# Optimization experiments

Measured on AMD Instinct MI355X. Metric: run time of the kernel, lower is better.

The kernel has to match this reference:

```python
import jax, jax.numpy as jnp
import numpy as np

B, C = 2000000, 24

def setup_inputs() -> dict:
    key = jax.random.key(0)
    k1, k2 = jax.random.split(key)
    input = jax.random.normal(k1, (B, C), dtype=jnp.float32)
    target = jax.random.randint(k2, (B, C), 0, 2, dtype=jnp.int32)
    return {"input": input, "target": target}

def reference(input, target):
    # LSEP: loss = log1p( sum_i sum_{p in pos_i, n in neg_i} exp(x_in - x_ip) ) / B
    # The ragged double loop factorizes per row:
    #   sum_{p,n} exp(x_n - x_p) = (sum_n exp(x_n)) * (sum_p exp(-x_p))
    pos = target > 0
    neg = target == 0
    s_neg = jnp.sum(jnp.where(neg, jnp.exp(input), 0.0), axis=1)   # [B]
    s_pos = jnp.sum(jnp.where(pos, jnp.exp(-input), 0.0), axis=1)  # [B]
    total = jnp.sum(s_neg * s_pos)
    batch_size = input.shape[0]
    return jnp.log1p(total) / batch_size
```

## Files before the change

### kernel.cpp

```cpp
#include <hip/hip_runtime.h>
#include <math.h>


constexpr int  ROWS    = 2000000;
constexpr int  HALVES  = ROWS * 2;
constexpr int  BLOCK   = 256;
constexpr int  GRID    = 3125;
constexpr int  THREADS = GRID * BLOCK;
constexpr int  ITERS   = HALVES / THREADS;

__global__ __launch_bounds__(BLOCK, 4) void lsep_main(
        const float4* __restrict__ input,
        const int4*   __restrict__ target,
        double*       __restrict__ partials)
{
    const int tid = blockIdx.x * BLOCK + threadIdx.x;

    double acc = 0.0;

    float4 xa0, xa1, xa2; int4 ta0, ta1, ta2;
    {
        const int f = 3 * tid;
        xa0 = input[f];  xa1 = input[f + 1];  xa2 = input[f + 2];
        ta0 = target[f]; ta1 = target[f + 1]; ta2 = target[f + 2];
    }

    int h = tid;
    #pragma unroll
    for (int i = 0; i < ITERS; ++i) {
        float4 xb0, xb1, xb2; int4 tb0, tb1, tb2;
        if (i + 1 < ITERS) {
            const int f = 3 * (h + THREADS);
            xb0 = input[f];  xb1 = input[f + 1];  xb2 = input[f + 2];
            tb0 = target[f]; tb1 = target[f + 1]; tb2 = target[f + 2];
        }

        float a = 0.0f, b = 0.0f, e;
        #define LSEP_ELEM(xc, tc) \
            e = __expf(tc > 0 ? -xc : xc); \
            if (tc > 0) b += e; else a += e;
        LSEP_ELEM(xa0.x, ta0.x) LSEP_ELEM(xa0.y, ta0.y) LSEP_ELEM(xa0.z, ta0.z) LSEP_ELEM(xa0.w, ta0.w)
        LSEP_ELEM(xa1.x, ta1.x) LSEP_ELEM(xa1.y, ta1.y) LSEP_ELEM(xa1.z, ta1.z) LSEP_ELEM(xa1.w, ta1.w)
        LSEP_ELEM(xa2.x, ta2.x) LSEP_ELEM(xa2.y, ta2.y) LSEP_ELEM(xa2.z, ta2.z) LSEP_ELEM(xa2.w, ta2.w)
        #undef LSEP_ELEM

        const float sa = a + __shfl_xor(a, 1, 64);
        const float sb = b + __shfl_xor(b, 1, 64);
        acc += (double)sa * (double)sb;

        xa0 = xb0; xa1 = xb1; xa2 = xb2;
        ta0 = tb0; ta1 = tb1; ta2 = tb2;
        h += THREADS;
    }

    __shared__ double sred[BLOCK / 64];
    #pragma unroll
    for (int off = 32; off > 0; off >>= 1)
        acc += __shfl_down(acc, off, 64);
    const int t = threadIdx.x;
    if ((t & 63) == 0) sred[t >> 6] = acc;
    __syncthreads();
    if (t == 0)
        partials[blockIdx.x] = (sred[0] + sred[1]) + (sred[2] + sred[3]);
}

__global__ void lsep_finalize(const double* __restrict__ partials,
                              float* __restrict__ out)
{
    __shared__ double sred[4];
    const int t = threadIdx.x;
    double s = 0.0;
    for (int i = t; i < GRID; i += 256) s += partials[i];
    #pragma unroll
    for (int off = 32; off > 0; off >>= 1)
        s += __shfl_down(s, off, 64);
    if ((t & 63) == 0) sred[t >> 6] = s;
    __syncthreads();
    if (t == 0) {
        const double total = ((sred[0] + sred[1]) + (sred[2] + sred[3])) * 0.5;
        out[0] = (float)(log1p(total) / (double)ROWS);
    }
}

extern "C" void kernel_launch(void* const* d_in, const int* in_sizes, int n_in,
                              void* d_out, int out_size, void* d_ws, size_t ws_size,
                              hipStream_t stream) {
    const float4* input  = (const float4*)d_in[0];
    const int4*   target = (const int4*)d_in[1];
    double*       ws     = (double*)d_ws;
    float*        out    = (float*)d_out;

    lsep_main<<<GRID, BLOCK, 0, stream>>>(input, target, ws);
    lsep_finalize<<<1, 256, 0, stream>>>(ws, out);
}
```

Before: 377.4 us.

## Coalesce loads by tile and rebuild per-row sums through shared memory

Each thread now loads consecutive float4s, so every wave reads contiguous lines instead of each thread reading a 48-byte strided chunk. Per-float4 partial sums go into a double-buffered shared array, and one thread per row combines them into that row's product. The sign flip and pos/neg selection are now branchless: an XOR on the sign bit and FMAs with a 0/1 mask. The grid-stride loop replaces the register prefetch and the pairwise shuffle, and the 0.5 correction is dropped. In exchange the kernel adds a barrier per tile, leaves only half the threads active in the row-combine step, and loses explicit prefetch.

```diff
diff --git a/kernel.cpp b/kernel.cpp
--- a/kernel.cpp
+++ b/kernel.cpp
@@ -2,62 +2,70 @@
 #include <math.h>
 
 
-constexpr int  ROWS    = 2000000;
-constexpr int  HALVES  = ROWS * 2;
-constexpr int  BLOCK   = 256;
-constexpr int  GRID    = 3125;
-constexpr int  THREADS = GRID * BLOCK;
-constexpr int  ITERS   = HALVES / THREADS;
+constexpr int  ROWS   = 2000000;
+constexpr int  BLOCK  = 256;
+constexpr int  GRID   = 2048;
+constexpr int  K      = 3;
+constexpr int  TILE4  = BLOCK * K;
+constexpr int  TROWS  = TILE4 / 6;
+constexpr int  NTILES = 15625;
 
-__global__ __launch_bounds__(BLOCK, 4) void lsep_main(
+__global__ __launch_bounds__(BLOCK) void lsep_main(
         const float4* __restrict__ input,
         const int4*   __restrict__ target,
         double*       __restrict__ partials)
 {
-    const int tid = blockIdx.x * BLOCK + threadIdx.x;
+    __shared__ float2 pair[2][TILE4];
+    __shared__ double sred[BLOCK / 64];
 
+    const int t = threadIdx.x;
     double acc = 0.0;
 
-    float4 xa0, xa1, xa2; int4 ta0, ta1, ta2;
-    {
-        const int f = 3 * tid;
-        xa0 = input[f];  xa1 = input[f + 1];  xa2 = input[f + 2];
-        ta0 = target[f]; ta1 = target[f + 1]; ta2 = target[f + 2];
+    int buf = 0;
+    for (int tile = blockIdx.x; tile < NTILES; tile += GRID, buf ^= 1) {
+        const long base = (long)tile * TILE4;
+
+        const float4 x0 = input[base + t];
+        const float4 x1 = input[base + t + BLOCK];
+        const float4 x2 = input[base + t + 2 * BLOCK];
+        const int4   g0 = target[base + t];
+        const int4   g1 = target[base + t + BLOCK];
+        const int4   g2 = target[base + t + 2 * BLOCK];
+
+        float2 p0, p1, p2;
+        #define LSEP_P4(dst, xv, tv) { \
+            float a_ = 0.0f, b_ = 0.0f; \
+            { const float e = __expf(__int_as_float(__float_as_int(xv.x) ^ (tv.x << 31))); \
+              const float f = (float)tv.x; b_ = fmaf(e, f, b_); a_ = fmaf(e, 1.0f - f, a_); } \
+            { const float e = __expf(__int_as_float(__float_as_int(xv.y) ^ (tv.y << 31))); \
+              const float f = (float)tv.y; b_ = fmaf(e, f, b_); a_ = fmaf(e, 1.0f - f, a_); } \
+            { const float e = __expf(__int_as_float(__float_as_int(xv.z) ^ (tv.z << 31))); \
+              const float f = (float)tv.z; b_ = fmaf(e, f, b_); a_ = fmaf(e, 1.0f - f, a_); } \
+            { const float e = __expf(__int_as_float(__float_as_int(xv.w) ^ (tv.w << 31))); \
+              const float f = (float)tv.w; b_ = fmaf(e, f, b_); a_ = fmaf(e, 1.0f - f, a_); } \
+            dst = make_float2(a_, b_); }
+        LSEP_P4(p0, x0, g0)
+        LSEP_P4(p1, x1, g1)
+        LSEP_P4(p2, x2, g2)
+        #undef LSEP_P4
+
+        pair[buf][t]             = p0;
+        pair[buf][t + BLOCK]     = p1;
+        pair[buf][t + 2 * BLOCK] = p2;
+        __syncthreads();
+
+        if (t < TROWS) {
+            const float4* pr = reinterpret_cast<const float4*>(pair[buf]) + 3 * t;
+            const float4 q0 = pr[0], q1 = pr[1], q2 = pr[2];
+            const float a = (q0.x + q0.z) + (q1.x + q1.z) + (q2.x + q2.z);
+            const float b = (q0.y + q0.w) + (q1.y + q1.w) + (q2.y + q2.w);
+            acc += (double)a * (double)b;
+        }
     }
 
-    int h = tid;
-    #pragma unroll
-    for (int i = 0; i < ITERS; ++i) {
-        float4 xb0, xb1, xb2; int4 tb0, tb1, tb2;
-        if (i + 1 < ITERS) {
-            const int f = 3 * (h + THREADS);
-            xb0 = input[f];  xb1 = input[f + 1];  xb2 = input[f + 2];
-            tb0 = target[f]; tb1 = target[f + 1]; tb2 = target[f + 2];
-        }
-
-        float a = 0.0f, b = 0.0f, e;
-        #define LSEP_ELEM(xc, tc) \
-            e = __expf(tc > 0 ? -xc : xc); \
-            if (tc > 0) b += e; else a += e;
-        LSEP_ELEM(xa0.x, ta0.x) LSEP_ELEM(xa0.y, ta0.y) LSEP_ELEM(xa0.z, ta0.z) LSEP_ELEM(xa0.w, ta0.w)
-        LSEP_ELEM(xa1.x, ta1.x) LSEP_ELEM(xa1.y, ta1.y) LSEP_ELEM(xa1.z, ta1.z) LSEP_ELEM(xa1.w, ta1.w)
-        LSEP_ELEM(xa2.x, ta2.x) LSEP_ELEM(xa2.y, ta2.y) LSEP_ELEM(xa2.z, ta2.z) LSEP_ELEM(xa2.w, ta2.w)
-        #undef LSEP_ELEM
-
-        const float sa = a + __shfl_xor(a, 1, 64);
-        const float sb = b + __shfl_xor(b, 1, 64);
-        acc += (double)sa * (double)sb;
-
-        xa0 = xb0; xa1 = xb1; xa2 = xb2;
-        ta0 = tb0; ta1 = tb1; ta2 = tb2;
-        h += THREADS;
-    }
-
-    __shared__ double sred[BLOCK / 64];
     #pragma unroll
     for (int off = 32; off > 0; off >>= 1)
         acc += __shfl_down(acc, off, 64);
-    const int t = threadIdx.x;
     if ((t & 63) == 0) sred[t >> 6] = acc;
     __syncthreads();
     if (t == 0)
@@ -76,10 +84,8 @@
         s += __shfl_down(s, off, 64);
     if ((t & 63) == 0) sred[t >> 6] = s;
     __syncthreads();
-    if (t == 0) {
-        const double total = ((sred[0] + sred[1]) + (sred[2] + sred[3])) * 0.5;
-        out[0] = (float)(log1p(total) / (double)ROWS);
-    }
+    if (t == 0)
+        out[0] = (float)(log1p((sred[0] + sred[1]) + (sred[2] + sred[3])) / (double)ROWS);
 }
 
 extern "C" void kernel_launch(void* const* d_in, const int* in_sizes, int n_in,
@@ -87,9 +93,9 @@
                               hipStream_t stream) {
     const float4* input  = (const float4*)d_in[0];
     const int4*   target = (const int4*)d_in[1];
-    double*       ws     = (double*)d_ws;
-    float*        out    = (float*)d_out;
+    double* partials = (double*)d_ws;
+    float*  out      = (float*)d_out;
 
-    lsep_main<<<GRID, BLOCK, 0, stream>>>(input, target, ws);
-    lsep_finalize<<<1, 256, 0, stream>>>(ws, out);
+    lsep_main<<<GRID, BLOCK, 0, stream>>>(input, target, partials);
+    lsep_finalize<<<1, 256, 0, stream>>>(partials, out);
 }
```

Measured after the change: 375.7 us. No clear change (-0.5%).
